# Kernel tuning notes

Hardware: AMD Instinct MI355X
Metric: run time of the kernel (lower is better)

## Reference

```python
import jax, jax.numpy as jnp
import numpy as np

B = 4096
N_DENSE = 13
N_SPARSE = 26
VOCAB = 100000
EMB = 8
CIN_SIZE = [26, 128, 128]


def setup_inputs() -> dict:
    key = jax.random.key(0)
    ks = jax.random.split(key, 24)
    s = 0.05
    dense = jax.random.normal(ks[0], (B, N_DENSE), dtype=jnp.float32)
    sparse = jax.random.randint(ks[1], (B, N_SPARSE), 0, VOCAB).astype(jnp.float32)
    inputs = jnp.concatenate([dense, sparse], axis=1)  # [B, 39]
    emb_tables = jax.random.normal(ks[2], (N_SPARSE, VOCAB, EMB), dtype=jnp.float32) * s
    linear_W = jax.random.normal(ks[3], (39, 1), dtype=jnp.float32) * s
    linear_b = jnp.zeros((1,), dtype=jnp.float32)
    # CIN Conv3d weights: kernel (H_prev, H0, 1) with out_channels H_next -> [H_next, H_prev, H0]
    W_cin0 = jax.random.normal(ks[4], (CIN_SIZE[1], CIN_SIZE[0], CIN_SIZE[0]), dtype=jnp.float32) * s
    b_cin0 = jnp.zeros((CIN_SIZE[1],), dtype=jnp.float32)
    W_cin1 = jax.random.normal(ks[5], (CIN_SIZE[2], CIN_SIZE[1], CIN_SIZE[0]), dtype=jnp.float32) * s
    b_cin1 = jnp.zeros((CIN_SIZE[2],), dtype=jnp.float32)
    cin_lin_W = jax.random.normal(ks[6], (256, 1), dtype=jnp.float32) * s
    cin_lin_b = jnp.zeros((1,), dtype=jnp.float32)
    d_W1 = jax.random.normal(ks[7], (221, 256), dtype=jnp.float32) * s
    d_b1 = jnp.zeros((256,), dtype=jnp.float32)
    d_W2 = jax.random.normal(ks[8], (256, 128), dtype=jnp.float32) * s
    d_b2 = jnp.zeros((128,), dtype=jnp.float32)
    d_W3 = jax.random.normal(ks[9], (128, 64), dtype=jnp.float32) * s
    d_b3 = jnp.zeros((64,), dtype=jnp.float32)
    d_W4 = jax.random.normal(ks[10], (64, 1), dtype=jnp.float32) * s
    d_b4 = jnp.zeros((1,), dtype=jnp.float32)
    return dict(inputs=inputs, emb_tables=emb_tables, linear_W=linear_W, linear_b=linear_b,
                W_cin0=W_cin0, b_cin0=b_cin0, W_cin1=W_cin1, b_cin1=b_cin1,
                cin_lin_W=cin_lin_W, cin_lin_b=cin_lin_b,
                d_W1=d_W1, d_b1=d_b1, d_W2=d_W2, d_b2=d_b2,
                d_W3=d_W3, d_b3=d_b3, d_W4=d_W4, d_b4=d_b4)


def reference(inputs, emb_tables, linear_W, linear_b,
              W_cin0, b_cin0, W_cin1, b_cin1, cin_lin_W, cin_lin_b,
              d_W1, d_b1, d_W2, d_b2, d_W3, d_b3, d_W4, d_b4):
    dense_in = inputs[:, :N_DENSE]                       # [B, 13]
    sparse_idx = inputs[:, N_DENSE:].astype(jnp.int32)   # [B, 26]

    # linear part over the raw inputs
    linear_out = inputs @ linear_W + linear_b            # [B, 1]

    # per-field embedding lookup: tables [F, V, E], idx [B, F] -> emb [B, F, E]
    emb = jax.vmap(lambda t, i: t[i], in_axes=(0, 1), out_axes=1)(emb_tables, sparse_idx)

    # CIN: each layer is an outer product over fields followed by a full-extent
    # Conv3d, i.e. X_{l+1}[b,o,k] = sum_{i,j} X_l[b,i,k] * X_0[b,j,k] * W[o,i,j] + b[o]
    X0 = emb
    Xi = emb
    res = []
    for W, b in ((W_cin0, b_cin0), (W_cin1, b_cin1)):
        Xi = jnp.einsum('bik,bjk,oij->bok', Xi, X0, W) + b[None, :, None]
        res.append(Xi)
    cin_feat = jnp.sum(jnp.concatenate(res, axis=1), axis=-1)  # [B, 256]
    cin_out = jax.nn.relu(cin_feat @ cin_lin_W + cin_lin_b)    # [B, 1]

    # dense MLP over [dense | flattened embeddings]
    h = jnp.concatenate([dense_in, emb.reshape(emb.shape[0], -1)], axis=1)  # [B, 221]
    h = jax.nn.relu(h @ d_W1 + d_b1)
    h = jax.nn.relu(h @ d_W2 + d_b2)
    h = jax.nn.relu(h @ d_W3 + d_b3)
    dense_out = jax.nn.relu(h @ d_W4 + d_b4)                   # [B, 1]

    return jax.nn.sigmoid(linear_out + cin_out + dense_out).reshape(-1)  # [B]
```

## Files before the change

kernel.cpp:

```cpp
#include <hip/hip_runtime.h>
#include <math.h>

#define B     4096
#define ND    13
#define NS    26
#define NF    39
#define VOCAB 100000
#define NP    351
#define NPP   360
#define CHP   45
#define GSTR  28
#define RPB   16
#define TPB   512
#define XSS   212

#define OFF_GST 0
#define OFF_CST 10080
#define OFF_C2J 10088

__global__ __launch_bounds__(256) void k_pre(const float* __restrict__ W0,
                                             const float* __restrict__ W1,
                                             const float* __restrict__ b0,
                                             const float* __restrict__ b1,
                                             const float* __restrict__ clw,
                                             float* __restrict__ Gst,
                                             float* __restrict__ cst,
                                             float* __restrict__ c2j) {
    int blk = blockIdx.x, tid = threadIdx.x;
    if (blk < 26) {
        int j = blk;
        __shared__ float vh[2][128];
        __shared__ float vj[128];
        __shared__ float c2r[2];
        {
            int i = tid & 127, h = tid >> 7;
            const float* wp = W1 + (long)(h * 64) * 3328 + i * 26 + j;
            float acc = 0.f;
#pragma unroll 8
            for (int o = 0; o < 64; o++) acc += clw[128 + h * 64 + o] * wp[o * 3328];
            vh[h][i] = acc;
        }
        __syncthreads();
        if (tid < 128) {
            float vv = vh[0][tid] + vh[1][tid];
            vj[tid] = vv;
            float c = vv * b0[tid];
            for (int off = 32; off; off >>= 1) c += __shfl_down(c, off, 64);
            if ((tid & 63) == 0) c2r[tid >> 6] = c;
        }
        __syncthreads();
        if (tid == 0) c2j[j] = c2r[0] + c2r[1];
        for (int p = tid; p < NPP; p += 256) {
            float g = 0.f;
            if (p < NP) {
                int l = 0, rem = p;
                while (rem >= NS - l) { rem -= NS - l; l++; }
                int m = l + rem;
                float sym = (l != m) ? 1.f : 0.f;
                const float* wa = W0 + l * 26 + m;
                const float* wb = W0 + m * 26 + l;
#pragma unroll 8
                for (int i = 0; i < 128; i++)
                    g += vj[i] * (wa[i * 676] + sym * wb[i * 676]);
            }
            Gst[p * GSTR + j] = g;
        }
    } else if (blk == 26) {
        for (int p = tid; p < NPP; p += 256) {
            float a = 0.f; int lmbits = 0;
            if (p < NP) {
                int l = 0, rem = p;
                while (rem >= NS - l) { rem -= NS - l; l++; }
                int m = l + rem;
                float sym = (l != m) ? 1.f : 0.f;
                const float* wa = W0 + l * 26 + m;
                const float* wb = W0 + m * 26 + l;
#pragma unroll 8
                for (int o = 0; o < 128; o++)
                    a += clw[o] * (wa[o * 676] + sym * wb[o * 676]);
                lmbits = (l << 5) | m;
            }
            Gst[p * GSTR + 26] = a;
            Gst[p * GSTR + 27] = __int_as_float(lmbits);
        }
    } else {
        __shared__ float red[2];
        float c = 0.f;
        if (tid < 128) {
            c = clw[tid] * b0[tid] + clw[128 + tid] * b1[tid];
            for (int off = 32; off; off >>= 1) c += __shfl_down(c, off, 64);
            if ((tid & 63) == 0) red[tid >> 6] = c;
        }
        __syncthreads();
        if (tid == 0) cst[0] = 8.f * (red[0] + red[1]);
    }
}

__global__ __launch_bounds__(512, 2) void k_main(
    const float* __restrict__ inputs, const float* __restrict__ tables,
    const float* __restrict__ lW, const float* __restrict__ lb,
    const float* __restrict__ Gst, const float* __restrict__ c2j,
    const float* __restrict__ cst,
    const float* __restrict__ dW1, const float* __restrict__ db1,
    const float* __restrict__ dW2, const float* __restrict__ db2,
    const float* __restrict__ dW3, const float* __restrict__ db3,
    const float* __restrict__ dW4, const float* __restrict__ db4,
    const float* __restrict__ clb,
    float* __restrict__ out) {
    __shared__ float4 sGst4[NPP * 7];
    __shared__ float insf[RPB][40];
    __shared__ float xs[RPB][XSS];
    __shared__ float inT[221][RPB];
    __shared__ float h1T[256][RPB];
    __shared__ float h2T[128][RPB];
    __shared__ float4 pbuf4[2048];
    __shared__ float lin_s[RPB], scin_s[RPB];
    __shared__ float redbuf[8][RPB];
    __shared__ float c2s[26];

    int tid = threadIdx.x;
    int b0r = blockIdx.x * RPB;

    for (int i = tid; i < NPP * 7; i += TPB) sGst4[i] = ((const float4*)Gst)[i];
    if (tid < 26) c2s[tid] = c2j[tid];
    for (int e = tid; e < RPB * NF; e += TPB) {
        int r = e / NF, c = e - r * NF;
        insf[r][c] = inputs[(b0r + r) * NF + c];
    }
    __syncthreads();

    if (tid < RPB * NS) {
        int r = tid / NS, f = tid - r * NS;
        int idx = (int)insf[r][ND + f];
        const float4* src = (const float4*)(tables + ((long)f * VOCAB + idx) * 8);
        float4 a = src[0], b4 = src[1];
        float4* dst = (float4*)&xs[r][f * 8];
        dst[0] = a; dst[1] = b4;
    }
    if (tid >= 448 && tid < 448 + RPB) {
        int r = tid - 448;
        float acc = lb[0];
        for (int c = 0; c < NF; c++) acc += insf[r][c] * lW[c];
        lin_s[r] = acc;
    }
    __syncthreads();

    for (int e = tid; e < 221 * RPB; e += TPB) {
        int c = e >> 4, r = e & 15;
        inT[c][r] = (c < ND) ? insf[r][c] : xs[r][c - ND];
    }

    {
        int lane = tid & 63, w = tid >> 6;
        int rlo = lane >> 3, k = lane & 7;
        const float4* grow = &sGst4[w * CHP * 7];
        float csel = (w == 0) ? 1.f : 0.f;
#pragma unroll 1
        for (int h = 0; h < 2; h++) {
            int row = (h << 3) + rlo;
            const float* xrow = &xs[row][0];
            float t[27];
#pragma unroll
            for (int j = 0; j < 27; j++) t[j] = 0.f;
#pragma unroll 2
            for (int pi = 0; pi < CHP; pi++) {
                float4 g6 = grow[pi * 7 + 6];
                int lm = __float_as_int(g6.w);
                float q = xrow[(lm >> 5) * 8 + k] * xrow[(lm & 31) * 8 + k];
                float4 g0 = grow[pi * 7 + 0], g1 = grow[pi * 7 + 1];
                float4 g2 = grow[pi * 7 + 2], g3 = grow[pi * 7 + 3];
                float4 g4 = grow[pi * 7 + 4], g5 = grow[pi * 7 + 5];
                t[0]  += g0.x * q; t[1]  += g0.y * q; t[2]  += g0.z * q; t[3]  += g0.w * q;
                t[4]  += g1.x * q; t[5]  += g1.y * q; t[6]  += g1.z * q; t[7]  += g1.w * q;
                t[8]  += g2.x * q; t[9]  += g2.y * q; t[10] += g2.z * q; t[11] += g2.w * q;
                t[12] += g3.x * q; t[13] += g3.y * q; t[14] += g3.z * q; t[15] += g3.w * q;
                t[16] += g4.x * q; t[17] += g4.y * q; t[18] += g4.z * q; t[19] += g4.w * q;
                t[20] += g5.x * q; t[21] += g5.y * q; t[22] += g5.z * q; t[23] += g5.w * q;
                t[24] += g6.x * q; t[25] += g6.y * q; t[26] += g6.z * q;
            }
            float part = t[26];
#pragma unroll
            for (int j = 0; j < 26; j++) {
                float xv = xrow[j * 8 + k];
                part += (t[j] + csel * c2s[j]) * xv;
            }
            part += __shfl_xor(part, 1, 64);
            part += __shfl_xor(part, 2, 64);
            part += __shfl_xor(part, 4, 64);
            if (k == 0) redbuf[w][row] = part;
        }
    }
    __syncthreads();

    if (tid < RPB) {
        float s = cst[0];
#pragma unroll
        for (int w = 0; w < 8; w++) s += redbuf[w][tid];
        scin_s[tid] = s;
    }
    {
        int o = tid & 255, cg = tid >> 8;
        int c0 = cg ? 111 : 0;
        int c1 = cg ? 221 : 111;
        float4 A0 = make_float4(0.f, 0.f, 0.f, 0.f);
        float4 A1 = A0, A2 = A0, A3 = A0;
#pragma unroll 4
        for (int c = c0; c < c1; c++) {
            float wv = dW1[c * 256 + o];
            const float4* ivp = (const float4*)&inT[c][0];
            float4 i0 = ivp[0], i1 = ivp[1], i2 = ivp[2], i3 = ivp[3];
            A0.x += i0.x * wv; A0.y += i0.y * wv; A0.z += i0.z * wv; A0.w += i0.w * wv;
            A1.x += i1.x * wv; A1.y += i1.y * wv; A1.z += i1.z * wv; A1.w += i1.w * wv;
            A2.x += i2.x * wv; A2.y += i2.y * wv; A2.z += i2.z * wv; A2.w += i2.w * wv;
            A3.x += i3.x * wv; A3.y += i3.y * wv; A3.z += i3.z * wv; A3.w += i3.w * wv;
        }
        int pb = (cg << 10) + (o << 2);
        pbuf4[pb + ((0 + o) & 3)] = A0;
        pbuf4[pb + ((1 + o) & 3)] = A1;
        pbuf4[pb + ((2 + o) & 3)] = A2;
        pbuf4[pb + ((3 + o) & 3)] = A3;
    }
    __syncthreads();
    if (tid < 256) {
        int o = tid, base = o << 2;
        float bb = db1[o];
        float4 S0, S1, S2, S3;
        {
            int s = (0 + o) & 3;
            float4 p = pbuf4[base + s], q = pbuf4[1024 + base + s];
            S0.x = fmaxf(p.x + q.x + bb, 0.f); S0.y = fmaxf(p.y + q.y + bb, 0.f);
            S0.z = fmaxf(p.z + q.z + bb, 0.f); S0.w = fmaxf(p.w + q.w + bb, 0.f);
        }
        {
            int s = (1 + o) & 3;
            float4 p = pbuf4[base + s], q = pbuf4[1024 + base + s];
            S1.x = fmaxf(p.x + q.x + bb, 0.f); S1.y = fmaxf(p.y + q.y + bb, 0.f);
            S1.z = fmaxf(p.z + q.z + bb, 0.f); S1.w = fmaxf(p.w + q.w + bb, 0.f);
        }
        {
            int s = (2 + o) & 3;
            float4 p = pbuf4[base + s], q = pbuf4[1024 + base + s];
            S2.x = fmaxf(p.x + q.x + bb, 0.f); S2.y = fmaxf(p.y + q.y + bb, 0.f);
            S2.z = fmaxf(p.z + q.z + bb, 0.f); S2.w = fmaxf(p.w + q.w + bb, 0.f);
        }
        {
            int s = (3 + o) & 3;
            float4 p = pbuf4[base + s], q = pbuf4[1024 + base + s];
            S3.x = fmaxf(p.x + q.x + bb, 0.f); S3.y = fmaxf(p.y + q.y + bb, 0.f);
            S3.z = fmaxf(p.z + q.z + bb, 0.f); S3.w = fmaxf(p.w + q.w + bb, 0.f);
        }
        *(float4*)&h1T[o][0]  = S0;
        *(float4*)&h1T[o][4]  = S1;
        *(float4*)&h1T[o][8]  = S2;
        *(float4*)&h1T[o][12] = S3;
    }
    __syncthreads();

    {
        int o = tid & 127, cg = tid >> 7;
        int c0 = cg << 6;
        float4 A0 = make_float4(0.f, 0.f, 0.f, 0.f);
        float4 A1 = A0, A2 = A0, A3 = A0;
#pragma unroll 4
        for (int cc = 0; cc < 64; cc++) {
            int c = c0 + cc;
            float wv = dW2[c * 128 + o];
            const float4* ivp = (const float4*)&h1T[c][0];
            float4 i0 = ivp[0], i1 = ivp[1], i2 = ivp[2], i3 = ivp[3];
            A0.x += i0.x * wv; A0.y += i0.y * wv; A0.z += i0.z * wv; A0.w += i0.w * wv;
            A1.x += i1.x * wv; A1.y += i1.y * wv; A1.z += i1.z * wv; A1.w += i1.w * wv;
            A2.x += i2.x * wv; A2.y += i2.y * wv; A2.z += i2.z * wv; A2.w += i2.w * wv;
            A3.x += i3.x * wv; A3.y += i3.y * wv; A3.z += i3.z * wv; A3.w += i3.w * wv;
        }
        int pb = (cg << 9) + (o << 2);
        pbuf4[pb + ((0 + o) & 3)] = A0;
        pbuf4[pb + ((1 + o) & 3)] = A1;
        pbuf4[pb + ((2 + o) & 3)] = A2;
        pbuf4[pb + ((3 + o) & 3)] = A3;
    }
    __syncthreads();
    if (tid < 128) {
        int o = tid, base = o << 2;
        float bb = db2[o];
        float4 S[4];
#pragma unroll
        for (int j = 0; j < 4; j++) {
            int s = (j + o) & 3;
            float sx = bb, sy = bb, sz = bb, sw = bb;
#pragma unroll
            for (int cg = 0; cg < 4; cg++) {
                float4 pv = pbuf4[(cg << 9) + base + s];
                sx += pv.x; sy += pv.y; sz += pv.z; sw += pv.w;
            }
            S[j].x = fmaxf(sx, 0.f); S[j].y = fmaxf(sy, 0.f);
            S[j].z = fmaxf(sz, 0.f); S[j].w = fmaxf(sw, 0.f);
        }
        *(float4*)&h2T[o][0]  = S[0];
        *(float4*)&h2T[o][4]  = S[1];
        *(float4*)&h2T[o][8]  = S[2];
        *(float4*)&h2T[o][12] = S[3];
    }
    __syncthreads();

    {
        int o = tid & 63, cg = tid >> 6;
        int c0 = cg << 4;
        float4 A0 = make_float4(0.f, 0.f, 0.f, 0.f);
        float4 A1 = A0, A2 = A0, A3 = A0;
#pragma unroll
        for (int cc = 0; cc < 16; cc++) {
            int c = c0 + cc;
            float wv = dW3[c * 64 + o];
            const float4* ivp = (const float4*)&h2T[c][0];
            float4 i0 = ivp[0], i1 = ivp[1], i2 = ivp[2], i3 = ivp[3];
            A0.x += i0.x * wv; A0.y += i0.y * wv; A0.z += i0.z * wv; A0.w += i0.w * wv;
            A1.x += i1.x * wv; A1.y += i1.y * wv; A1.z += i1.z * wv; A1.w += i1.w * wv;
            A2.x += i2.x * wv; A2.y += i2.y * wv; A2.z += i2.z * wv; A2.w += i2.w * wv;
            A3.x += i3.x * wv; A3.y += i3.y * wv; A3.z += i3.z * wv; A3.w += i3.w * wv;
        }
        int pb = (cg << 8) + (o << 2);
        pbuf4[pb + ((0 + o) & 3)] = A0;
        pbuf4[pb + ((1 + o) & 3)] = A1;
        pbuf4[pb + ((2 + o) & 3)] = A2;
        pbuf4[pb + ((3 + o) & 3)] = A3;
    }
    __syncthreads();

    if (tid < 64) {
        int o = tid, base = o << 2;
        float4 S0 = make_float4(0.f, 0.f, 0.f, 0.f);
        float4 S1 = S0, S2 = S0, S3 = S0;
#pragma unroll
        for (int cg = 0; cg < 8; cg++) {
            int pb = (cg << 8) + base;
            float4 p0 = pbuf4[pb + ((0 + o) & 3)];
            float4 p1 = pbuf4[pb + ((1 + o) & 3)];
            float4 p2 = pbuf4[pb + ((2 + o) & 3)];
            float4 p3 = pbuf4[pb + ((3 + o) & 3)];
            S0.x += p0.x; S0.y += p0.y; S0.z += p0.z; S0.w += p0.w;
            S1.x += p1.x; S1.y += p1.y; S1.z += p1.z; S1.w += p1.w;
            S2.x += p2.x; S2.y += p2.y; S2.z += p2.z; S2.w += p2.w;
            S3.x += p3.x; S3.y += p3.y; S3.z += p3.z; S3.w += p3.w;
        }
        float b3 = db3[o], w4 = dW4[o];
        S0.x = fmaxf(S0.x + b3, 0.f) * w4; S0.y = fmaxf(S0.y + b3, 0.f) * w4;
        S0.z = fmaxf(S0.z + b3, 0.f) * w4; S0.w = fmaxf(S0.w + b3, 0.f) * w4;
        S1.x = fmaxf(S1.x + b3, 0.f) * w4; S1.y = fmaxf(S1.y + b3, 0.f) * w4;
        S1.z = fmaxf(S1.z + b3, 0.f) * w4; S1.w = fmaxf(S1.w + b3, 0.f) * w4;
        S2.x = fmaxf(S2.x + b3, 0.f) * w4; S2.y = fmaxf(S2.y + b3, 0.f) * w4;
        S2.z = fmaxf(S2.z + b3, 0.f) * w4; S2.w = fmaxf(S2.w + b3, 0.f) * w4;
        S3.x = fmaxf(S3.x + b3, 0.f) * w4; S3.y = fmaxf(S3.y + b3, 0.f) * w4;
        S3.z = fmaxf(S3.z + b3, 0.f) * w4; S3.w = fmaxf(S3.w + b3, 0.f) * w4;
#pragma unroll
        for (int off = 1; off < 64; off <<= 1) {
            S0.x += __shfl_xor(S0.x, off, 64); S0.y += __shfl_xor(S0.y, off, 64);
            S0.z += __shfl_xor(S0.z, off, 64); S0.w += __shfl_xor(S0.w, off, 64);
            S1.x += __shfl_xor(S1.x, off, 64); S1.y += __shfl_xor(S1.y, off, 64);
            S1.z += __shfl_xor(S1.z, off, 64); S1.w += __shfl_xor(S1.w, off, 64);
            S2.x += __shfl_xor(S2.x, off, 64); S2.y += __shfl_xor(S2.y, off, 64);
            S2.z += __shfl_xor(S2.z, off, 64); S2.w += __shfl_xor(S2.w, off, 64);
            S3.x += __shfl_xor(S3.x, off, 64); S3.y += __shfl_xor(S3.y, off, 64);
            S3.z += __shfl_xor(S3.z, off, 64); S3.w += __shfl_xor(S3.w, off, 64);
        }
        if (tid == 0) {
            float sv[16] = { S0.x, S0.y, S0.z, S0.w, S1.x, S1.y, S1.z, S1.w,
                             S2.x, S2.y, S2.z, S2.w, S3.x, S3.y, S3.z, S3.w };
            float bb = db4[0], cb = clb[0];
#pragma unroll
            for (int r = 0; r < RPB; r++) {
                float dense = fmaxf(sv[r] + bb, 0.f);
                float cin = fmaxf(scin_s[r] + cb, 0.f);
                float x = lin_s[r] + cin + dense;
                out[b0r + r] = 1.f / (1.f + expf(-x));
            }
        }
    }
}

extern "C" void kernel_launch(void* const* d_in, const int* in_sizes, int n_in,
                              void* d_out, int out_size, void* d_ws, size_t ws_size,
                              hipStream_t stream) {
    const float* inputs = (const float*)d_in[0];
    const float* tables = (const float*)d_in[1];
    const float* lW     = (const float*)d_in[2];
    const float* lb     = (const float*)d_in[3];
    const float* W0     = (const float*)d_in[4];
    const float* b0     = (const float*)d_in[5];
    const float* W1c    = (const float*)d_in[6];
    const float* b1c    = (const float*)d_in[7];
    const float* clw    = (const float*)d_in[8];
    const float* clb    = (const float*)d_in[9];
    const float* dW1    = (const float*)d_in[10];
    const float* db1    = (const float*)d_in[11];
    const float* dW2    = (const float*)d_in[12];
    const float* db2    = (const float*)d_in[13];
    const float* dW3    = (const float*)d_in[14];
    const float* db3    = (const float*)d_in[15];
    const float* dW4    = (const float*)d_in[16];
    const float* db4    = (const float*)d_in[17];

    float* ws   = (float*)d_ws;
    float* Gst  = ws + OFF_GST;
    float* cst  = ws + OFF_CST;
    float* c2j  = ws + OFF_C2J;

    k_pre<<<28, 256, 0, stream>>>(W0, W1c, b0, b1c, clw, Gst, cst, c2j);
    k_main<<<B / RPB, TPB, 0, stream>>>(inputs, tables, lW, lb, Gst, c2j, cst,
                                        dW1, db1, dW2, db2, dW3, db3, dW4, db4, clb,
                                        (float*)d_out);
}
```

Measured before the change: 214.7 us.

## Halve rows per block and alias MLP scratch onto Gst LDS buffer

Rows per block drop from 16 to 8, doubling the grid, and the launch bound now asks for 4 blocks per CU. The MLP scratch buffers (partial sums and h1/h2 activations) are overlaid on the Gst shared buffer, which is no longer needed after the CIN stage. The CIN loop becomes a single pass, and the MLP stages keep two float4 accumulators instead of four. The aim is more resident waves per CU and better latency hiding. The cost is that every block rereads Gst and the dense weight matrices, which doubles weight traffic through L2, and each block gets less weight reuse across rows.

Result: faster. 210.4 us (-2.0%).

```diff
diff --git a/kernel.cpp b/kernel.cpp
--- a/kernel.cpp
+++ b/kernel.cpp
@@ -10,7 +10,7 @@
 #define NPP   360
 #define CHP   45
 #define GSTR  28
-#define RPB   16
+#define RPB   8
 #define TPB   512
 #define XSS   212
 
@@ -96,7 +96,7 @@
     }
 }
 
-__global__ __launch_bounds__(512, 2) void k_main(
+__global__ __launch_bounds__(512, 4) void k_main(
     const float* __restrict__ inputs, const float* __restrict__ tables,
     const float* __restrict__ lW, const float* __restrict__ lb,
     const float* __restrict__ Gst, const float* __restrict__ c2j,
@@ -111,12 +111,13 @@
     __shared__ float insf[RPB][40];
     __shared__ float xs[RPB][XSS];
     __shared__ float inT[221][RPB];
-    __shared__ float h1T[256][RPB];
-    __shared__ float h2T[128][RPB];
-    __shared__ float4 pbuf4[2048];
     __shared__ float lin_s[RPB], scin_s[RPB];
     __shared__ float redbuf[8][RPB];
     __shared__ float c2s[26];
+
+    float4* pbuf4 = sGst4;
+    float*  h1T   = (float*)(sGst4 + 1024);
+    float*  h2T   = (float*)(sGst4 + 1536);
 
     int tid = threadIdx.x;
     int b0r = blockIdx.x * RPB;
@@ -146,49 +147,45 @@
     __syncthreads();
 
     for (int e = tid; e < 221 * RPB; e += TPB) {
-        int c = e >> 4, r = e & 15;
+        int c = e >> 3, r = e & 7;
         inT[c][r] = (c < ND) ? insf[r][c] : xs[r][c - ND];
     }
 
     {
         int lane = tid & 63, w = tid >> 6;
-        int rlo = lane >> 3, k = lane & 7;
+        int row = lane >> 3, k = lane & 7;
         const float4* grow = &sGst4[w * CHP * 7];
         float csel = (w == 0) ? 1.f : 0.f;
-#pragma unroll 1
-        for (int h = 0; h < 2; h++) {
-            int row = (h << 3) + rlo;
-            const float* xrow = &xs[row][0];
-            float t[27];
-#pragma unroll
-            for (int j = 0; j < 27; j++) t[j] = 0.f;
+        const float* xrow = &xs[row][0];
+        float t[27];
+#pragma unroll
+        for (int j = 0; j < 27; j++) t[j] = 0.f;
 #pragma unroll 2
-            for (int pi = 0; pi < CHP; pi++) {
-                float4 g6 = grow[pi * 7 + 6];
-                int lm = __float_as_int(g6.w);
-                float q = xrow[(lm >> 5) * 8 + k] * xrow[(lm & 31) * 8 + k];
-                float4 g0 = grow[pi * 7 + 0], g1 = grow[pi * 7 + 1];
-                float4 g2 = grow[pi * 7 + 2], g3 = grow[pi * 7 + 3];
-                float4 g4 = grow[pi * 7 + 4], g5 = grow[pi * 7 + 5];
-                t[0]  += g0.x * q; t[1]  += g0.y * q; t[2]  += g0.z * q; t[3]  += g0.w * q;
-                t[4]  += g1.x * q; t[5]  += g1.y * q; t[6]  += g1.z * q; t[7]  += g1.w * q;
-                t[8]  += g2.x * q; t[9]  += g2.y * q; t[10] += g2.z * q; t[11] += g2.w * q;
-                t[12] += g3.x * q; t[13] += g3.y * q; t[14] += g3.z * q; t[15] += g3.w * q;
-                t[16] += g4.x * q; t[17] += g4.y * q; t[18] += g4.z * q; t[19] += g4.w * q;
-                t[20] += g5.x * q; t[21] += g5.y * q; t[22] += g5.z * q; t[23] += g5.w * q;
-                t[24] += g6.x * q; t[25] += g6.y * q; t[26] += g6.z * q;
-            }
-            float part = t[26];
-#pragma unroll
-            for (int j = 0; j < 26; j++) {
-                float xv = xrow[j * 8 + k];
-                part += (t[j] + csel * c2s[j]) * xv;
-            }
-            part += __shfl_xor(part, 1, 64);
-            part += __shfl_xor(part, 2, 64);
-            part += __shfl_xor(part, 4, 64);
-            if (k == 0) redbuf[w][row] = part;
-        }
+        for (int pi = 0; pi < CHP; pi++) {
+            float4 g6 = grow[pi * 7 + 6];
+            int lm = __float_as_int(g6.w);
+            float q = xrow[(lm >> 5) * 8 + k] * xrow[(lm & 31) * 8 + k];
+            float4 g0 = grow[pi * 7 + 0], g1 = grow[pi * 7 + 1];
+            float4 g2 = grow[pi * 7 + 2], g3 = grow[pi * 7 + 3];
+            float4 g4 = grow[pi * 7 + 4], g5 = grow[pi * 7 + 5];
+            t[0]  += g0.x * q; t[1]  += g0.y * q; t[2]  += g0.z * q; t[3]  += g0.w * q;
+            t[4]  += g1.x * q; t[5]  += g1.y * q; t[6]  += g1.z * q; t[7]  += g1.w * q;
+            t[8]  += g2.x * q; t[9]  += g2.y * q; t[10] += g2.z * q; t[11] += g2.w * q;
+            t[12] += g3.x * q; t[13] += g3.y * q; t[14] += g3.z * q; t[15] += g3.w * q;
+            t[16] += g4.x * q; t[17] += g4.y * q; t[18] += g4.z * q; t[19] += g4.w * q;
+            t[20] += g5.x * q; t[21] += g5.y * q; t[22] += g5.z * q; t[23] += g5.w * q;
+            t[24] += g6.x * q; t[25] += g6.y * q; t[26] += g6.z * q;
+        }
+        float part = t[26];
+#pragma unroll
+        for (int j = 0; j < 26; j++) {
+            float xv = xrow[j * 8 + k];
+            part += (t[j] + csel * c2s[j]) * xv;
+        }
+        part += __shfl_xor(part, 1, 64);
+        part += __shfl_xor(part, 2, 64);
+        part += __shfl_xor(part, 4, 64);
+        if (k == 0) redbuf[w][row] = part;
     }
     __syncthreads();
 
@@ -203,56 +200,31 @@
         int c0 = cg ? 111 : 0;
         int c1 = cg ? 221 : 111;
         float4 A0 = make_float4(0.f, 0.f, 0.f, 0.f);
-        float4 A1 = A0, A2 = A0, A3 = A0;
+        float4 A1 = A0;
 #pragma unroll 4
         for (int c = c0; c < c1; c++) {
             float wv = dW1[c * 256 + o];
             const float4* ivp = (const float4*)&inT[c][0];
-            float4 i0 = ivp[0], i1 = ivp[1], i2 = ivp[2], i3 = ivp[3];
+            float4 i0 = ivp[0], i1 = ivp[1];
             A0.x += i0.x * wv; A0.y += i0.y * wv; A0.z += i0.z * wv; A0.w += i0.w * wv;
             A1.x += i1.x * wv; A1.y += i1.y * wv; A1.z += i1.z * wv; A1.w += i1.w * wv;
-            A2.x += i2.x * wv; A2.y += i2.y * wv; A2.z += i2.z * wv; A2.w += i2.w * wv;
-            A3.x += i3.x * wv; A3.y += i3.y * wv; A3.z += i3.z * wv; A3.w += i3.w * wv;
-        }
-        int pb = (cg << 10) + (o << 2);
-        pbuf4[pb + ((0 + o) & 3)] = A0;
-        pbuf4[pb + ((1 + o) & 3)] = A1;
-        pbuf4[pb + ((2 + o) & 3)] = A2;
-        pbuf4[pb + ((3 + o) & 3)] = A3;
+        }
+        pbuf4[cg * 512 + 0 * 256 + o] = A0;
+        pbuf4[cg * 512 + 1 * 256 + o] = A1;
     }
     __syncthreads();
     if (tid < 256) {
-        int o = tid, base = o << 2;
+        int o = tid;
         float bb = db1[o];
-        float4 S0, S1, S2, S3;
-        {
-            int s = (0 + o) & 3;
-            float4 p = pbuf4[base + s], q = pbuf4[1024 + base + s];
-            S0.x = fmaxf(p.x + q.x + bb, 0.f); S0.y = fmaxf(p.y + q.y + bb, 0.f);
-            S0.z = fmaxf(p.z + q.z + bb, 0.f); S0.w = fmaxf(p.w + q.w + bb, 0.f);
-        }
-        {
-            int s = (1 + o) & 3;
-            float4 p = pbuf4[base + s], q = pbuf4[1024 + base + s];
-            S1.x = fmaxf(p.x + q.x + bb, 0.f); S1.y = fmaxf(p.y + q.y + bb, 0.f);
-            S1.z = fmaxf(p.z + q.z + bb, 0.f); S1.w = fmaxf(p.w + q.w + bb, 0.f);
-        }
-        {
-            int s = (2 + o) & 3;
-            float4 p = pbuf4[base + s], q = pbuf4[1024 + base + s];
-            S2.x = fmaxf(p.x + q.x + bb, 0.f); S2.y = fmaxf(p.y + q.y + bb, 0.f);
-            S2.z = fmaxf(p.z + q.z + bb, 0.f); S2.w = fmaxf(p.w + q.w + bb, 0.f);
-        }
-        {
-            int s = (3 + o) & 3;
-            float4 p = pbuf4[base + s], q = pbuf4[1024 + base + s];
-            S3.x = fmaxf(p.x + q.x + bb, 0.f); S3.y = fmaxf(p.y + q.y + bb, 0.f);
-            S3.z = fmaxf(p.z + q.z + bb, 0.f); S3.w = fmaxf(p.w + q.w + bb, 0.f);
-        }
-        *(float4*)&h1T[o][0]  = S0;
-        *(float4*)&h1T[o][4]  = S1;
-        *(float4*)&h1T[o][8]  = S2;
-        *(float4*)&h1T[o][12] = S3;
+        float4 p0 = pbuf4[o],       q0 = pbuf4[512 + o];
+        float4 p1 = pbuf4[256 + o], q1 = pbuf4[768 + o];
+        float4 S0, S1;
+        S0.x = fmaxf(p0.x + q0.x + bb, 0.f); S0.y = fmaxf(p0.y + q0.y + bb, 0.f);
+        S0.z = fmaxf(p0.z + q0.z + bb, 0.f); S0.w = fmaxf(p0.w + q0.w + bb, 0.f);
+        S1.x = fmaxf(p1.x + q1.x + bb, 0.f); S1.y = fmaxf(p1.y + q1.y + bb, 0.f);
+        S1.z = fmaxf(p1.z + q1.z + bb, 0.f); S1.w = fmaxf(p1.w + q1.w + bb, 0.f);
+        *(float4*)&h1T[o * 8]     = S0;
+        *(float4*)&h1T[o * 8 + 4] = S1;
     }
     __syncthreads();
 
@@ -260,45 +232,39 @@
         int o = tid & 127, cg = tid >> 7;
         int c0 = cg << 6;
         float4 A0 = make_float4(0.f, 0.f, 0.f, 0.f);
-        float4 A1 = A0, A2 = A0, A3 = A0;
+        float4 A1 = A0;
 #pragma unroll 4
         for (int cc = 0; cc < 64; cc++) {
             int c = c0 + cc;
             float wv = dW2[c * 128 + o];
-            const float4* ivp = (const float4*)&h1T[c][0];
-            float4 i0 = ivp[0], i1 = ivp[1], i2 = ivp[2], i3 = ivp[3];
+            const float4* ivp = (const float4*)&h1T[c * 8];
+            float4 i0 = ivp[0], i1 = ivp[1];
             A0.x += i0.x * wv; A0.y += i0.y * wv; A0.z += i0.z * wv; A0.w += i0.w * wv;
             A1.x += i1.x * wv; A1.y += i1.y * wv; A1.z += i1.z * wv; A1.w += i1.w * wv;
-            A2.x += i2.x * wv; A2.y += i2.y * wv; A2.z += i2.z * wv; A2.w += i2.w * wv;
-            A3.x += i3.x * wv; A3.y += i3.y * wv; A3.z += i3.z * wv; A3.w += i3.w * wv;
-        }
-        int pb = (cg << 9) + (o << 2);
-        pbuf4[pb + ((0 + o) & 3)] = A0;
-        pbuf4[pb + ((1 + o) & 3)] = A1;
-        pbuf4[pb + ((2 + o) & 3)] = A2;
-        pbuf4[pb + ((3 + o) & 3)] = A3;
+        }
+        pbuf4[cg * 256 + 0 * 128 + o] = A0;
+        pbuf4[cg * 256 + 1 * 128 + o] = A1;
     }
     __syncthreads();
     if (tid < 128) {
-        int o = tid, base = o << 2;
+        int o = tid;
         float bb = db2[o];
-        float4 S[4];
-#pragma unroll
-        for (int j = 0; j < 4; j++) {
-            int s = (j + o) & 3;
-            float sx = bb, sy = bb, sz = bb, sw = bb;
-#pragma unroll
-            for (int cg = 0; cg < 4; cg++) {
-                float4 pv = pbuf4[(cg << 9) + base + s];
-                sx += pv.x; sy += pv.y; sz += pv.z; sw += pv.w;
-            }
-            S[j].x = fmaxf(sx, 0.f); S[j].y = fmaxf(sy, 0.f);
-            S[j].z = fmaxf(sz, 0.f); S[j].w = fmaxf(sw, 0.f);
-        }
-        *(float4*)&h2T[o][0]  = S[0];
-        *(float4*)&h2T[o][4]  = S[1];
-        *(float4*)&h2T[o][8]  = S[2];
-        *(float4*)&h2T[o][12] = S[3];
+        float sx0 = bb, sy0 = bb, sz0 = bb, sw0 = bb;
+        float sx1 = bb, sy1 = bb, sz1 = bb, sw1 = bb;
+#pragma unroll
+        for (int cg = 0; cg < 4; cg++) {
+            float4 p0 = pbuf4[cg * 256 + o];
+            float4 p1 = pbuf4[cg * 256 + 128 + o];
+            sx0 += p0.x; sy0 += p0.y; sz0 += p0.z; sw0 += p0.w;
+            sx1 += p1.x; sy1 += p1.y; sz1 += p1.z; sw1 += p1.w;
+        }
+        float4 S0, S1;
+        S0.x = fmaxf(sx0, 0.f); S0.y = fmaxf(sy0, 0.f);
+        S0.z = fmaxf(sz0, 0.f); S0.w = fmaxf(sw0, 0.f);
+        S1.x = fmaxf(sx1, 0.f); S1.y = fmaxf(sy1, 0.f);
+        S1.z = fmaxf(sz1, 0.f); S1.w = fmaxf(sw1, 0.f);
+        *(float4*)&h2T[o * 8]     = S0;
+        *(float4*)&h2T[o * 8 + 4] = S1;
     }
     __syncthreads();
 
@@ -306,65 +272,46 @@
         int o = tid & 63, cg = tid >> 6;
         int c0 = cg << 4;
         float4 A0 = make_float4(0.f, 0.f, 0.f, 0.f);
-        float4 A1 = A0, A2 = A0, A3 = A0;
-#pragma unroll
+        float4 A1 = A0;
+#pragma unroll 8
         for (int cc = 0; cc < 16; cc++) {
             int c = c0 + cc;
             float wv = dW3[c * 64 + o];
-            const float4* ivp = (const float4*)&h2T[c][0];
-            float4 i0 = ivp[0], i1 = ivp[1], i2 = ivp[2], i3 = ivp[3];
+            const float4* ivp = (const float4*)&h2T[c * 8];
+            float4 i0 = ivp[0], i1 = ivp[1];
             A0.x += i0.x * wv; A0.y += i0.y * wv; A0.z += i0.z * wv; A0.w += i0.w * wv;
             A1.x += i1.x * wv; A1.y += i1.y * wv; A1.z += i1.z * wv; A1.w += i1.w * wv;
-            A2.x += i2.x * wv; A2.y += i2.y * wv; A2.z += i2.z * wv; A2.w += i2.w * wv;
-            A3.x += i3.x * wv; A3.y += i3.y * wv; A3.z += i3.z * wv; A3.w += i3.w * wv;
-        }
-        int pb = (cg << 8) + (o << 2);
-        pbuf4[pb + ((0 + o) & 3)] = A0;
-        pbuf4[pb + ((1 + o) & 3)] = A1;
-        pbuf4[pb + ((2 + o) & 3)] = A2;
-        pbuf4[pb + ((3 + o) & 3)] = A3;
+        }
+        pbuf4[cg * 128 + 0 * 64 + o] = A0;
+        pbuf4[cg * 128 + 1 * 64 + o] = A1;
     }
     __syncthreads();
 
     if (tid < 64) {
-        int o = tid, base = o << 2;
+        int o = tid;
         float4 S0 = make_float4(0.f, 0.f, 0.f, 0.f);
-        float4 S1 = S0, S2 = S0, S3 = S0;
+        float4 S1 = S0;
 #pragma unroll
         for (int cg = 0; cg < 8; cg++) {
-            int pb = (cg << 8) + base;
-            float4 p0 = pbuf4[pb + ((0 + o) & 3)];
-            float4 p1 = pbuf4[pb + ((1 + o) & 3)];
-            float4 p2 = pbuf4[pb + ((2 + o) & 3)];
-            float4 p3 = pbuf4[pb + ((3 + o) & 3)];
+            float4 p0 = pbuf4[cg * 128 + o];
+            float4 p1 = pbuf4[cg * 128 + 64 + o];
             S0.x += p0.x; S0.y += p0.y; S0.z += p0.z; S0.w += p0.w;
             S1.x += p1.x; S1.y += p1.y; S1.z += p1.z; S1.w += p1.w;
-            S2.x += p2.x; S2.y += p2.y; S2.z += p2.z; S2.w += p2.w;
-            S3.x += p3.x; S3.y += p3.y; S3.z += p3.z; S3.w += p3.w;
         }
         float b3 = db3[o], w4 = dW4[o];
         S0.x = fmaxf(S0.x + b3, 0.f) * w4; S0.y = fmaxf(S0.y + b3, 0.f) * w4;
         S0.z = fmaxf(S0.z + b3, 0.f) * w4; S0.w = fmaxf(S0.w + b3, 0.f) * w4;
         S1.x = fmaxf(S1.x + b3, 0.f) * w4; S1.y = fmaxf(S1.y + b3, 0.f) * w4;
         S1.z = fmaxf(S1.z + b3, 0.f) * w4; S1.w = fmaxf(S1.w + b3, 0.f) * w4;
-        S2.x = fmaxf(S2.x + b3, 0.f) * w4; S2.y = fmaxf(S2.y + b3, 0.f) * w4;
-        S2.z = fmaxf(S2.z + b3, 0.f) * w4; S2.w = fmaxf(S2.w + b3, 0.f) * w4;
-        S3.x = fmaxf(S3.x + b3, 0.f) * w4; S3.y = fmaxf(S3.y + b3, 0.f) * w4;
-        S3.z = fmaxf(S3.z + b3, 0.f) * w4; S3.w = fmaxf(S3.w + b3, 0.f) * w4;
 #pragma unroll
         for (int off = 1; off < 64; off <<= 1) {
             S0.x += __shfl_xor(S0.x, off, 64); S0.y += __shfl_xor(S0.y, off, 64);
             S0.z += __shfl_xor(S0.z, off, 64); S0.w += __shfl_xor(S0.w, off, 64);
             S1.x += __shfl_xor(S1.x, off, 64); S1.y += __shfl_xor(S1.y, off, 64);
             S1.z += __shfl_xor(S1.z, off, 64); S1.w += __shfl_xor(S1.w, off, 64);
-            S2.x += __shfl_xor(S2.x, off, 64); S2.y += __shfl_xor(S2.y, off, 64);
-            S2.z += __shfl_xor(S2.z, off, 64); S2.w += __shfl_xor(S2.w, off, 64);
-            S3.x += __shfl_xor(S3.x, off, 64); S3.y += __shfl_xor(S3.y, off, 64);
-            S3.z += __shfl_xor(S3.z, off, 64); S3.w += __shfl_xor(S3.w, off, 64);
         }
         if (tid == 0) {
-            float sv[16] = { S0.x, S0.y, S0.z, S0.w, S1.x, S1.y, S1.z, S1.w,
-                             S2.x, S2.y, S2.z, S2.w, S3.x, S3.y, S3.z, S3.w };
+            float sv[8] = { S0.x, S0.y, S0.z, S0.w, S1.x, S1.y, S1.z, S1.w };
             float bb = db4[0], cb = clb[0];
 #pragma unroll
             for (int r = 0; r < RPB; r++) {
```
